# Performance work log

Measured on AMD Instinct MI355X. Metric: run time of the kernel, lower is better.

The kernel has to match this reference:

```python
import jax, jax.numpy as jnp
import numpy as np

NEG_BIG = -9e15
ALPHA = 0.2  # leaky relu slope


def setup_inputs() -> dict:
    key = jax.random.key(0)
    k1, k2, k3, k4 = jax.random.split(key, 4)
    B, N, Fin, Fout = 8, 2048, 128, 64
    h = jax.random.normal(k1, (B, N, Fin), dtype=jnp.float32)
    adj = jax.random.randint(k2, (B, N, N), 0, 2, dtype=jnp.int32)
    # xavier_uniform-like init scale
    W = jax.random.uniform(k3, (Fin, Fout), dtype=jnp.float32, minval=-1.0, maxval=1.0) * (1.414 * np.sqrt(6.0 / (Fin + Fout)))
    a = jax.random.uniform(k4, (2 * Fout, 1), dtype=jnp.float32, minval=-1.0, maxval=1.0) * (1.414 * np.sqrt(6.0 / (2 * Fout + 1)))
    return {"h": h, "adj": adj, "W": W, "a": a}


def reference(h, adj, W, a):
    # h: [B,N,Fin], adj: [B,N,N], W: [Fin,Fout], a: [2*Fout,1]
    Fout = W.shape[1]
    Wh = jnp.einsum('bni,io->bno', h, W)            # [B,N,Fout]
    # e_ij = leakyrelu(a[:Fout] . Wh_i + a[Fout:] . Wh_j)  (decomposed, same math
    # as the original concat + matmul with a)
    f_src = Wh @ a[:Fout, 0]                        # [B,N]
    f_dst = Wh @ a[Fout:, 0]                        # [B,N]
    e = f_src[:, :, None] + f_dst[:, None, :]       # [B,N,N]
    e = jnp.where(e > 0, e, ALPHA * e)              # leaky relu
    e = jnp.where(adj > 0, e, NEG_BIG)              # mask
    attention = jax.nn.softmax(e, axis=2)           # [B,N,N]
    h_prime = jnp.einsum('bnm,bmo->bno', attention, Wh)
    return jax.nn.elu(h_prime)
```

## Files before the change

### kernel.cpp

```cpp
#include <hip/hip_runtime.h>
#include <hip/hip_bf16.h>

constexpr int Bb  = 8;
constexpr int Nn  = 2048;
constexpr int FIN = 128;
constexpr int FOUT = 64;
constexpr float LOG2E = 1.4426950408889634f;

typedef __bf16 bf16x8 __attribute__((ext_vector_type(8)));
typedef __bf16 bf16x2 __attribute__((ext_vector_type(2)));
typedef float  f32x4  __attribute__((ext_vector_type(4)));
typedef int    i32x4  __attribute__((ext_vector_type(4)));
typedef unsigned int u32;

__device__ __forceinline__ u32 f2bf_bits(float f) {
    u32 u = __builtin_bit_cast(u32, f);
    return (u + 0x7FFFu + ((u >> 16) & 1u)) >> 16;
}

__global__ __launch_bounds__(256) void gat_k1(
        const float* __restrict__ h, const float* __restrict__ W,
        const float* __restrict__ a, __bf16* __restrict__ whfrag,
        float* __restrict__ fs, float* __restrict__ fd) {
    const int blk = blockIdx.x;
    const int b   = blk >> 6;
    const int t32 = blk & 63;
    const int n0  = t32 * 32;
    const int l   = threadIdx.x & 63;
    const int w   = __builtin_amdgcn_readfirstlane((int)(threadIdx.x >> 6));

    const float a0 = a[l];
    const float a1 = a[FOUT + l];

    float acc[8];
#pragma unroll
    for (int r = 0; r < 8; ++r) acc[r] = 0.f;

    const float* hbase = h + (size_t)(b * Nn + n0 + w * 8) * FIN;

#pragma unroll 1
    for (int c0 = 0; c0 < FIN; c0 += 32) {
        float wreg[32];
#pragma unroll
        for (int cc = 0; cc < 32; ++cc) wreg[cc] = W[(c0 + cc) * FOUT + l];
#pragma unroll
        for (int r = 0; r < 8; ++r) {
            const float* hrow = hbase + r * FIN + c0;
#pragma unroll
            for (int cc = 0; cc < 32; ++cc) acc[r] = fmaf(hrow[cc], wreg[cc], acc[r]);
        }
    }

#pragma unroll
    for (int r = 0; r < 8; ++r) {
        float s0 = acc[r] * a0;
        float s1 = acc[r] * a1;
#pragma unroll
        for (int off = 32; off >= 1; off >>= 1) {
            s0 += __shfl_xor(s0, off, 64);
            s1 += __shfl_xor(s1, off, 64);
        }
        if (l == 0) {
            fs[b * Nn + n0 + w * 8 + r] = s0 * LOG2E;
            fd[b * Nn + n0 + w * 8 + r] = s1 * LOG2E;
        }
    }

    u32 pk[4];
#pragma unroll
    for (int i = 0; i < 4; ++i)
        pk[i] = f2bf_bits(acc[2 * i]) | (f2bf_bits(acc[2 * i + 1]) << 16);
    const int slotg = ((b * 64 + t32) * 4 + (l >> 4)) * 64 + ((w << 4) | (l & 15));
    reinterpret_cast<uint4*>(whfrag)[slotg] = make_uint4(pk[0], pk[1], pk[2], pk[3]);
}

__global__ __launch_bounds__(256, 4) void gat_k2(
        const int* __restrict__ adj, const __bf16* __restrict__ whfrag,
        const float* __restrict__ fs, const float* __restrict__ fd,
        float* __restrict__ out) {
    const int blk = blockIdx.x;
    const int b   = blk >> 7;
    const int i0  = (blk & 127) * 16;
    const int l   = threadIdx.x & 63;
    const int w   = __builtin_amdgcn_readfirstlane((int)(threadIdx.x >> 6));

    __shared__ __align__(16) char  aLDS[4 * 4096];
    __shared__ f32x4 comb[4][4][64];
    __shared__ float zpart[4][16];

    const int g  = l >> 4;
    const int jc = l & 15;

    char* myA = aLDS + w * 4096;

    float fs_loc[4];
#pragma unroll
    for (int rr = 0; rr < 4; ++rr) fs_loc[rr] = fs[b * Nn + i0 + g * 4 + rr];

    const float* fdp  = fd + b * Nn + w * 64 + jc * 4;
    const int*   adj0 = adj + (size_t)(b * Nn + i0 + g * 4) * Nn + w * 64 + jc * 4;

    const bf16x8* bfr = reinterpret_cast<const bf16x8*>(whfrag)
                        + (size_t)(b * 256) * 64 + l;

    f32x4 acc[4] = {{0,0,0,0},{0,0,0,0},{0,0,0,0},{0,0,0,0}};
    f32x4 accz   = {0.f, 0.f, 0.f, 0.f};

    bf16x8 onesv;
#pragma unroll
    for (int i = 0; i < 8; ++i) onesv[i] = (__bf16)1.0f;

    i32x4 adjQ[2][4];
    f32x4 fdQ[2];

#pragma unroll
    for (int rr = 0; rr < 4; ++rr)
        adjQ[0][rr] = *reinterpret_cast<const i32x4*>(adj0 + (size_t)rr * Nn);
    fdQ[0] = *reinterpret_cast<const f32x4*>(fdp);

#pragma unroll 2
    for (int it = 0; it < 8; ++it) {
        const int cur = it & 1, nxt = cur ^ 1;
        if (it < 7) {
#pragma unroll
            for (int rr = 0; rr < 4; ++rr)
                adjQ[nxt][rr] = *reinterpret_cast<const i32x4*>(
                                    adj0 + (size_t)rr * Nn + (it + 1) * 256);
            fdQ[nxt] = *reinterpret_cast<const f32x4*>(fdp + (it + 1) * 256);
        }

        char* buf = myA + cur * 2048;
#pragma unroll
        for (int rr = 0; rr < 4; ++rr) {
            const int row = g * 4 + rr;
            u32 wds[2];
#pragma unroll
            for (int hp = 0; hp < 2; ++hp) {
                float pv[2];
#pragma unroll
                for (int q = 0; q < 2; ++q) {
                    const int jj = hp * 2 + q;
                    float e  = fs_loc[rr] + fdQ[cur][jj];
                    float lr = fmaxf(e, 0.2f * e);
                    float p  = exp2f(lr);
                    pv[q] = (adjQ[cur][rr][jj] > 0) ? p : 0.f;
                }
                wds[hp] = __builtin_bit_cast(u32,
                            (bf16x2){(__bf16)pv[0], (__bf16)pv[1]});
            }
            const int boff = (row * 128 + jc * 8) ^ ((row & 7) << 4);
            *reinterpret_cast<uint2*>(buf + boff) = make_uint2(wds[0], wds[1]);
        }

        asm volatile("s_waitcnt lgkmcnt(0)" ::: "memory");
        __builtin_amdgcn_sched_barrier(0x20);

        {
            const int rb0 = (((l & 15) * 128 + 0 * 64 + g * 16) ^ ((l & 7) << 4));
            bf16x8 av = *reinterpret_cast<const bf16x8*>(buf + rb0);
#pragma unroll
            for (int o16 = 0; o16 < 4; ++o16)
                acc[o16] = __builtin_amdgcn_mfma_f32_16x16x32_bf16(
                               av, bfr[(((it * 8 + w * 2 + 0) * 4) + o16) * 64], acc[o16], 0, 0, 0);
            accz = __builtin_amdgcn_mfma_f32_16x16x32_bf16(av, onesv, accz, 0, 0, 0);
        }
        {
            const int rb1 = (((l & 15) * 128 + 1 * 64 + g * 16) ^ ((l & 7) << 4));
            bf16x8 av = *reinterpret_cast<const bf16x8*>(buf + rb1);
#pragma unroll
            for (int o16 = 0; o16 < 4; ++o16)
                acc[o16] = __builtin_amdgcn_mfma_f32_16x16x32_bf16(
                               av, bfr[(((it * 8 + w * 2 + 1) * 4) + o16) * 64], acc[o16], 0, 0, 0);
            accz = __builtin_amdgcn_mfma_f32_16x16x32_bf16(av, onesv, accz, 0, 0, 0);
        }
    }

    if ((l & 15) == 0) {
#pragma unroll
        for (int r = 0; r < 4; ++r) zpart[w][(l >> 4) * 4 + r] = accz[r];
    }
#pragma unroll
    for (int o16 = 0; o16 < 4; ++o16) comb[w][o16][l] = acc[o16];
    __syncthreads();

    f32x4 res = comb[0][w][l];
#pragma unroll
    for (int wp = 1; wp < 4; ++wp) res += comb[wp][w][l];

#pragma unroll
    for (int r = 0; r < 4; ++r) {
        const int row = g * 4 + r;
        float z = zpart[0][row] + zpart[1][row] + zpart[2][row] + zpart[3][row];
        float v = res[r] / z;
        v = v > 0.f ? v : expm1f(v);
        out[(size_t)(b * Nn + i0 + row) * FOUT + w * 16 + jc] = v;
    }
}

extern "C" void kernel_launch(void* const* d_in, const int* in_sizes, int n_in,
                              void* d_out, int out_size, void* d_ws, size_t ws_size,
                              hipStream_t stream) {
    const float* h   = (const float*)d_in[0];
    const int*   adj = (const int*)d_in[1];
    const float* W   = (const float*)d_in[2];
    const float* a   = (const float*)d_in[3];
    float* out = (float*)d_out;

    __bf16* whfrag = (__bf16*)d_ws;
    float*  fs     = (float*)((char*)d_ws + (size_t)Bb * Nn * FOUT * 2);
    float*  fd     = fs + Bb * Nn;

    gat_k1<<<dim3(Bb * 64), dim3(256), 0, stream>>>(h, W, a, whfrag, fs, fd);
    gat_k2<<<dim3(Bb * 128), dim3(256), 0, stream>>>(adj, whfrag, fs, fd, out);
}
```

Baseline: 51.26 us.

## Stage h rows in LDS in k1 and give each k2 wave a contiguous column range

In the first kernel, each block now copies its 32 rows of h into shared memory with coalesced float4 loads before the FMA loop, so the per-lane scalar global reads of h are gone. In the second kernel, each wave now handles a contiguous 512-column slice of adj and reads 32 lanes × 16 bytes per row over two rows at a time, with a larger LDS staging buffer and four MFMA k-blocks per iteration. The aim is longer contiguous adj reads from DRAM and fewer loop iterations. The cost is more registers and LDS per block, and launch bounds drop to 3 blocks per SM, which lowers occupancy.

```diff
diff --git a/kernel.cpp b/kernel.cpp
--- a/kernel.cpp
+++ b/kernel.cpp
@@ -29,14 +29,25 @@
     const int l   = threadIdx.x & 63;
     const int w   = __builtin_amdgcn_readfirstlane((int)(threadIdx.x >> 6));
 
+    __shared__ __align__(16) float hT[32][FIN];
+
+    {
+        const float4* hb = reinterpret_cast<const float4*>(h + (size_t)(b * Nn + n0) * FIN);
+        float4* dst = reinterpret_cast<float4*>(&hT[0][0]);
+#pragma unroll
+        for (int k = 0; k < 4; ++k) {
+            const int flat = threadIdx.x + k * 256;
+            dst[flat] = hb[flat];
+        }
+    }
+    __syncthreads();
+
     const float a0 = a[l];
     const float a1 = a[FOUT + l];
 
     float acc[8];
 #pragma unroll
     for (int r = 0; r < 8; ++r) acc[r] = 0.f;
-
-    const float* hbase = h + (size_t)(b * Nn + n0 + w * 8) * FIN;
 
 #pragma unroll 1
     for (int c0 = 0; c0 < FIN; c0 += 32) {
@@ -45,9 +56,10 @@
         for (int cc = 0; cc < 32; ++cc) wreg[cc] = W[(c0 + cc) * FOUT + l];
 #pragma unroll
         for (int r = 0; r < 8; ++r) {
-            const float* hrow = hbase + r * FIN + c0;
-#pragma unroll
-            for (int cc = 0; cc < 32; ++cc) acc[r] = fmaf(hrow[cc], wreg[cc], acc[r]);
+            const int row = w * 8 + r;
+#pragma unroll
+            for (int cc = 0; cc < 32; ++cc)
+                acc[r] = fmaf(hT[row][c0 + cc], wreg[cc], acc[r]);
         }
     }
 
@@ -74,7 +86,7 @@
     reinterpret_cast<uint4*>(whfrag)[slotg] = make_uint4(pk[0], pk[1], pk[2], pk[3]);
 }
 
-__global__ __launch_bounds__(256, 4) void gat_k2(
+__global__ __launch_bounds__(256, 3) void gat_k2(
         const int* __restrict__ adj, const __bf16* __restrict__ whfrag,
         const float* __restrict__ fs, const float* __restrict__ fd,
         float* __restrict__ out) {
@@ -84,21 +96,24 @@
     const int l   = threadIdx.x & 63;
     const int w   = __builtin_amdgcn_readfirstlane((int)(threadIdx.x >> 6));
 
-    __shared__ __align__(16) char  aLDS[4 * 4096];
+    __shared__ __align__(16) char  aLDS[4 * 8192];
     __shared__ f32x4 comb[4][4][64];
     __shared__ float zpart[4][16];
 
+    const int hi = l >> 5;
+    const int lo = l & 31;
     const int g  = l >> 4;
     const int jc = l & 15;
 
-    char* myA = aLDS + w * 4096;
-
-    float fs_loc[4];
-#pragma unroll
-    for (int rr = 0; rr < 4; ++rr) fs_loc[rr] = fs[b * Nn + i0 + g * 4 + rr];
-
-    const float* fdp  = fd + b * Nn + w * 64 + jc * 4;
-    const int*   adj0 = adj + (size_t)(b * Nn + i0 + g * 4) * Nn + w * 64 + jc * 4;
+    char* myA = aLDS + w * 8192;
+
+    float fs_loc[8];
+#pragma unroll
+    for (int t = 0; t < 8; ++t) fs_loc[t] = fs[b * Nn + i0 + 2 * t + hi];
+
+    const int    jq0  = w * 512;
+    const float* fdp  = fd + b * Nn + jq0 + lo * 4;
+    const int*   adj0 = adj + (size_t)(b * Nn + i0 + hi) * Nn + jq0 + lo * 4;
 
     const bf16x8* bfr = reinterpret_cast<const bf16x8*>(whfrag)
                         + (size_t)(b * 256) * 64 + l;
@@ -110,67 +125,56 @@
 #pragma unroll
     for (int i = 0; i < 8; ++i) onesv[i] = (__bf16)1.0f;
 
-    i32x4 adjQ[2][4];
+    i32x4 adjT[2][8];
     f32x4 fdQ[2];
 
 #pragma unroll
-    for (int rr = 0; rr < 4; ++rr)
-        adjQ[0][rr] = *reinterpret_cast<const i32x4*>(adj0 + (size_t)rr * Nn);
+    for (int t = 0; t < 8; ++t)
+        adjT[0][t] = *reinterpret_cast<const i32x4*>(adj0 + (size_t)(2 * t) * Nn);
     fdQ[0] = *reinterpret_cast<const f32x4*>(fdp);
 
 #pragma unroll 2
-    for (int it = 0; it < 8; ++it) {
+    for (int it = 0; it < 4; ++it) {
         const int cur = it & 1, nxt = cur ^ 1;
-        if (it < 7) {
-#pragma unroll
-            for (int rr = 0; rr < 4; ++rr)
-                adjQ[nxt][rr] = *reinterpret_cast<const i32x4*>(
-                                    adj0 + (size_t)rr * Nn + (it + 1) * 256);
-            fdQ[nxt] = *reinterpret_cast<const f32x4*>(fdp + (it + 1) * 256);
-        }
-
-        char* buf = myA + cur * 2048;
-#pragma unroll
-        for (int rr = 0; rr < 4; ++rr) {
-            const int row = g * 4 + rr;
-            u32 wds[2];
-#pragma unroll
-            for (int hp = 0; hp < 2; ++hp) {
-                float pv[2];
-#pragma unroll
-                for (int q = 0; q < 2; ++q) {
-                    const int jj = hp * 2 + q;
-                    float e  = fs_loc[rr] + fdQ[cur][jj];
-                    float lr = fmaxf(e, 0.2f * e);
-                    float p  = exp2f(lr);
-                    pv[q] = (adjQ[cur][rr][jj] > 0) ? p : 0.f;
-                }
-                wds[hp] = __builtin_bit_cast(u32,
-                            (bf16x2){(__bf16)pv[0], (__bf16)pv[1]});
+        if (it < 3) {
+#pragma unroll
+            for (int t = 0; t < 8; ++t)
+                adjT[nxt][t] = *reinterpret_cast<const i32x4*>(
+                                   adj0 + (size_t)(2 * t) * Nn + (it + 1) * 128);
+            fdQ[nxt] = *reinterpret_cast<const f32x4*>(fdp + (it + 1) * 128);
+        }
+
+        char* buf = myA + cur * 4096;
+#pragma unroll
+        for (int t = 0; t < 8; ++t) {
+            const int row = 2 * t + hi;
+            float pv[4];
+#pragma unroll
+            for (int q = 0; q < 4; ++q) {
+                float e  = fs_loc[t] + fdQ[cur][q];
+                float lr = fmaxf(e, 0.2f * e);
+                float p  = exp2f(lr);
+                pv[q] = (adjT[cur][t][q] > 0) ? p : 0.f;
             }
-            const int boff = (row * 128 + jc * 8) ^ ((row & 7) << 4);
-            *reinterpret_cast<uint2*>(buf + boff) = make_uint2(wds[0], wds[1]);
+            u32 w0 = __builtin_bit_cast(u32, (bf16x2){(__bf16)pv[0], (__bf16)pv[1]});
+            u32 w1 = __builtin_bit_cast(u32, (bf16x2){(__bf16)pv[2], (__bf16)pv[3]});
+            const int boff = (row * 256 + lo * 8) ^ ((row & 7) << 4);
+            *reinterpret_cast<uint2*>(buf + boff) = make_uint2(w0, w1);
         }
 
         asm volatile("s_waitcnt lgkmcnt(0)" ::: "memory");
         __builtin_amdgcn_sched_barrier(0x20);
 
-        {
-            const int rb0 = (((l & 15) * 128 + 0 * 64 + g * 16) ^ ((l & 7) << 4));
-            bf16x8 av = *reinterpret_cast<const bf16x8*>(buf + rb0);
+#pragma unroll
+        for (int kb = 0; kb < 4; ++kb) {
+            const int rbyte = (((l & 15) * 256 + kb * 64 + (l >> 4) * 16)
+                               ^ ((l & 7) << 4));
+            bf16x8 av = *reinterpret_cast<const bf16x8*>(buf + rbyte);
+            const int t32 = w * 16 + it * 4 + kb;
 #pragma unroll
             for (int o16 = 0; o16 < 4; ++o16)
                 acc[o16] = __builtin_amdgcn_mfma_f32_16x16x32_bf16(
-                               av, bfr[(((it * 8 + w * 2 + 0) * 4) + o16) * 64], acc[o16], 0, 0, 0);
-            accz = __builtin_amdgcn_mfma_f32_16x16x32_bf16(av, onesv, accz, 0, 0, 0);
-        }
-        {
-            const int rb1 = (((l & 15) * 128 + 1 * 64 + g * 16) ^ ((l & 7) << 4));
-            bf16x8 av = *reinterpret_cast<const bf16x8*>(buf + rb1);
-#pragma unroll
-            for (int o16 = 0; o16 < 4; ++o16)
-                acc[o16] = __builtin_amdgcn_mfma_f32_16x16x32_bf16(
-                               av, bfr[(((it * 8 + w * 2 + 1) * 4) + o16) * 64], acc[o16], 0, 0, 0);
+                               av, bfr[(t32 * 4 + o16) * 64], acc[o16], 0, 0, 0);
             accz = __builtin_amdgcn_mfma_f32_16x16x32_bf16(av, onesv, accz, 0, 0, 0);
         }
     }
```

New measurement: 55.59 us. 1.08x slower.
